# Performance work log

Hardware: AMD Instinct MI355X
Metric: run time of the kernel (lower is better)

## Reference

```python
import jax, jax.numpy as jnp
import numpy as np

NUM_LAYERS = 6
D_MODEL = 256
N_HEADS = 8
N_LEVELS = 4
N_POINTS = 4
D_FFN = 1024
HEAD_DIM = D_MODEL // N_HEADS
B = 2
NQ = 1600
SPATIAL = np.array([[64, 64], [32, 32], [16, 16], [8, 8]], dtype=np.int64)  # (H_l, W_l)
LEVEL_START = np.concatenate([[0], np.cumsum(SPATIAL.prod(1))[:-1]]).astype(np.int64)
S_TOTAL = int(SPATIAL.prod(1).sum())  # 5440


def layer_norm(x, g, b, eps=1e-5):
    mu = x.mean(-1, keepdims=True)
    var = ((x - mu) ** 2).mean(-1, keepdims=True)
    return (x - mu) * jax.lax.rsqrt(var + eps) * g + b


def mha(q, k, v, wq, bq, wk, bk, wv, bv, wo, bo):
    # torch nn.MultiheadAttention math (dropout=eval identity)
    Bb, N, d = q.shape
    def proj(x, w, bias):
        return (x @ w.T + bias).reshape(Bb, -1, N_HEADS, HEAD_DIM).transpose(0, 2, 1, 3)
    qh, kh, vh = proj(q, wq, bq), proj(k, wk, bk), proj(v, wv, bv)
    scores = jnp.einsum('bhqd,bhkd->bhqk', qh, kh) / np.float32(np.sqrt(HEAD_DIM))
    attn = jax.nn.softmax(scores, axis=-1)
    out = jnp.einsum('bhqk,bhkd->bhqd', attn, vh).transpose(0, 2, 1, 3).reshape(Bb, N, d)
    return out @ wo.T + bo


def ms_deform_attn(query, ref_points, src, w_off, b_off, w_attn, b_attn, w_val, b_val, w_out, b_out):
    Bb, Nq, d = query.shape
    value = (src @ w_val.T + b_val).reshape(Bb, -1, N_HEADS, HEAD_DIM)  # [B,S,H,D]
    off = (query @ w_off.T + b_off).reshape(Bb, Nq, N_HEADS, N_LEVELS, N_POINTS, 2)
    aw = (query @ w_attn.T + b_attn).reshape(Bb, Nq, N_HEADS, N_LEVELS * N_POINTS)
    aw = jax.nn.softmax(aw, -1).reshape(Bb, Nq, N_HEADS, N_LEVELS, N_POINTS)
    # offset normalizer is (W_l, H_l)
    norm = jnp.asarray(SPATIAL[:, ::-1].copy(), dtype=query.dtype)  # [L,2]
    loc = ref_points[:, :, None, :, None, :] + off / norm[None, None, None, :, None, :]
    out = jnp.zeros((Bb, Nq, N_HEADS, HEAD_DIM), query.dtype)
    for l in range(N_LEVELS):
        Hl, Wl = int(SPATIAL[l, 0]), int(SPATIAL[l, 1])
        s0 = int(LEVEL_START[l])
        v_l = value[:, s0:s0 + Hl * Wl].transpose(0, 2, 1, 3)  # [B,H,S_l,D]
        loc_l = loc[:, :, :, l]  # [B,Nq,H,P,2]
        # grid_sample bilinear, align_corners=False, padding zeros
        x = loc_l[..., 0] * Wl - 0.5
        y = loc_l[..., 1] * Hl - 0.5
        x0 = jnp.floor(x)
        y0 = jnp.floor(y)
        wx1 = x - x0
        wy1 = y - y0
        samp = jnp.zeros((Bb, Nq, N_HEADS, N_POINTS, HEAD_DIM), query.dtype)
        for dy, wy in ((0, 1.0 - wy1), (1, wy1)):
            for dx, wx in ((0, 1.0 - wx1), (1, wx1)):
                xi = x0 + dx
                yi = y0 + dy
                valid = ((xi >= 0) & (xi <= Wl - 1) & (yi >= 0) & (yi <= Hl - 1)).astype(query.dtype)
                xi_c = jnp.clip(xi, 0, Wl - 1).astype(jnp.int32)
                yi_c = jnp.clip(yi, 0, Hl - 1).astype(jnp.int32)
                idx = (yi_c * Wl + xi_c).transpose(0, 2, 1, 3).reshape(Bb, N_HEADS, Nq * N_POINTS)
                g = jnp.take_along_axis(v_l, idx[..., None], axis=2)  # [B,H,Nq*P,D]
                g = g.reshape(Bb, N_HEADS, Nq, N_POINTS, HEAD_DIM).transpose(0, 2, 1, 3, 4)
                samp = samp + g * (wx * wy * valid)[..., None]
        out = out + (samp * aw[:, :, :, l, :, None]).sum(3)
    return out.reshape(Bb, Nq, d) @ w_out.T + b_out


def decoder_forward(tgt, query_pos, reference_points, src, params):
    out = tgt
    for i in range(NUM_LAYERS):
        p = {k: v[i] for k, v in params.items()}
        q = out + query_pos
        t2 = mha(q, q, out, p['sa_w_q'], p['sa_b_q'], p['sa_w_k'], p['sa_b_k'],
                 p['sa_w_v'], p['sa_b_v'], p['sa_w_o'], p['sa_b_o'])
        out = layer_norm(out + t2, p['ln2_g'], p['ln2_b'])
        t2 = ms_deform_attn(out + query_pos, reference_points, src,
                            p['ca_w_off'], p['ca_b_off'], p['ca_w_attn'], p['ca_b_attn'],
                            p['ca_w_val'], p['ca_b_val'], p['ca_w_out'], p['ca_b_out'])
        out = out + t2
        out = layer_norm(out, p['ln1_g'], p['ln1_b'])
        t2 = jax.nn.relu(out @ p['ffn_w1'].T + p['ffn_b1']) @ p['ffn_w2'].T + p['ffn_b2']
        out = layer_norm(out + t2, p['ln3_g'], p['ln3_b'])
    return out


PARAM_NAMES = ['sa_w_q', 'sa_b_q', 'sa_w_k', 'sa_b_k', 'sa_w_v', 'sa_b_v', 'sa_w_o', 'sa_b_o',
               'ln2_g', 'ln2_b',
               'ca_w_off', 'ca_b_off', 'ca_w_attn', 'ca_b_attn', 'ca_w_val', 'ca_b_val',
               'ca_w_out', 'ca_b_out', 'ln1_g', 'ln1_b',
               'ffn_w1', 'ffn_b1', 'ffn_w2', 'ffn_b2', 'ln3_g', 'ln3_b']


def setup_inputs() -> dict:
    key = jax.random.key(0)
    ks = jax.random.split(key, 64)
    d = D_MODEL
    HLP = N_HEADS * N_LEVELS * N_POINTS
    shapes = {
        'sa_w_q': (d, d), 'sa_b_q': (d,), 'sa_w_k': (d, d), 'sa_b_k': (d,),
        'sa_w_v': (d, d), 'sa_b_v': (d,), 'sa_w_o': (d, d), 'sa_b_o': (d,),
        'ca_w_off': (HLP * 2, d), 'ca_b_off': (HLP * 2,),
        'ca_w_attn': (HLP, d), 'ca_b_attn': (HLP,),
        'ca_w_val': (d, d), 'ca_b_val': (d,),
        'ca_w_out': (d, d), 'ca_b_out': (d,),
        'ffn_w1': (D_FFN, d), 'ffn_b1': (D_FFN,),
        'ffn_w2': (d, D_FFN), 'ffn_b2': (D_FFN * 0 + d,) if False else (d,),
    }
    inp = {}
    inp['tgt'] = jax.random.normal(ks[0], (B, NQ, d), jnp.float32)
    inp['query_pos'] = jax.random.normal(ks[1], (B, NQ, d), jnp.float32)
    inp['reference_points'] = jax.random.uniform(ks[2], (B, NQ, N_LEVELS, 2), jnp.float32)
    inp['src'] = jax.random.normal(ks[3], (B, S_TOTAL, d), jnp.float32)
    i = 4
    for name in PARAM_NAMES:
        if name.startswith('ln'):
            if name.endswith('_g'):
                inp[name] = jnp.ones((NUM_LAYERS, d), jnp.float32)
            else:
                inp[name] = jnp.zeros((NUM_LAYERS, d), jnp.float32)
        else:
            shp = (NUM_LAYERS,) + shapes[name]
            inp[name] = jax.random.normal(ks[i], shp, jnp.float32) * 0.02
            i += 1
    inp['src_spatial_shapes'] = jnp.asarray(SPATIAL)
    inp['src_level_start_index'] = jnp.asarray(LEVEL_START)
    return inp


def reference(tgt, query_pos, reference_points, src,
              sa_w_q, sa_b_q, sa_w_k, sa_b_k, sa_w_v, sa_b_v, sa_w_o, sa_b_o,
              ln2_g, ln2_b,
              ca_w_off, ca_b_off, ca_w_attn, ca_b_attn, ca_w_val, ca_b_val,
              ca_w_out, ca_b_out, ln1_g, ln1_b,
              ffn_w1, ffn_b1, ffn_w2, ffn_b2, ln3_g, ln3_b,
              src_spatial_shapes, src_level_start_index):
    params = dict(zip(PARAM_NAMES, (sa_w_q, sa_b_q, sa_w_k, sa_b_k, sa_w_v, sa_b_v, sa_w_o, sa_b_o,
                                    ln2_g, ln2_b, ca_w_off, ca_b_off, ca_w_attn, ca_b_attn,
                                    ca_w_val, ca_b_val, ca_w_out, ca_b_out, ln1_g, ln1_b,
                                    ffn_w1, ffn_b1, ffn_w2, ffn_b2, ln3_g, ln3_b)))
    return decoder_forward(tgt, query_pos, reference_points, src, params)
```

## Files before the change

kernel.cpp:

```cpp
#include <hip/hip_runtime.h>

#define D_MODEL   256
#define NQ        1600
#define BATCH     2
#define NHEAD     8
#define HDIM      32
#define S_TOTAL   5440
#define D_FFN     1024
#define NUM_LAYERS 6

#define M_Q   (BATCH * NQ)
#define M_V   (BATCH * S_TOTAL)
#define ROW_ELEMS ((size_t)M_Q * D_MODEL)

using short8  = __attribute__((ext_vector_type(8))) short;
using floatx4 = __attribute__((ext_vector_type(4))) float;

__device__ __forceinline__ ushort f2bf(float f) {
    union { float f; unsigned u; } x; x.f = f;
    unsigned r = (x.u + 0x7fffu + ((x.u >> 16) & 1u)) >> 16;
    return (ushort)r;
}
__device__ __forceinline__ ushort f2bf_trunc(float f) {
    union { float f; unsigned u; } x; x.f = f;
    return (ushort)(x.u >> 16);
}
__device__ __forceinline__ float bf2f(ushort b) {
    union { unsigned u; float f; } x; x.u = ((unsigned)b) << 16;
    return x.f;
}

struct GSeg {
    const ushort* A;
    const ushort* W;
    const float*  bias;
    void*         C;
    int           ldc;
    int           mode;
    int           mblk;
    float         scale;
};
struct GArgs { GSeg s[16]; };

__global__ __launch_bounds__(256) void gemm_multi(GArgs args, int K)
{
    const GSeg sg = args.s[blockIdx.y];
    if ((int)blockIdx.x >= sg.mblk) return;
    __shared__ ushort Al[64][40];
    __shared__ ushort Bl[64][40];
    const int tid  = threadIdx.x;
    const int bm   = blockIdx.x * 64;
    const int lr   = tid >> 2;
    const int lc   = tid & 3;
    const int wave = tid >> 6;
    const int lane = tid & 63;
    const int mo   = (wave & 1) * 32;
    const int no   = (wave >> 1) * 32;
    const int row16 = lane & 15;
    const int quad  = lane >> 4;

    floatx4 acc[2][2] = {};

    const ushort* aG = sg.A + (size_t)(bm + lr) * K + lc * 8;
    const ushort* wG = sg.W + (size_t)lr * K + lc * 8;

    for (int k0 = 0; k0 < K; k0 += 32) {
        __syncthreads();
        *(short8*)&Al[lr][lc * 8] = *(const short8*)(aG + k0);
        *(short8*)&Bl[lr][lc * 8] = *(const short8*)(wG + k0);
        __syncthreads();
        short8 af0 = *(const short8*)&Al[mo + row16][quad * 8];
        short8 af1 = *(const short8*)&Al[mo + 16 + row16][quad * 8];
        short8 bf0 = *(const short8*)&Bl[no + row16][quad * 8];
        short8 bf1 = *(const short8*)&Bl[no + 16 + row16][quad * 8];
        acc[0][0] = __builtin_amdgcn_mfma_f32_16x16x32_bf16(af0, bf0, acc[0][0], 0, 0, 0);
        acc[0][1] = __builtin_amdgcn_mfma_f32_16x16x32_bf16(af0, bf1, acc[0][1], 0, 0, 0);
        acc[1][0] = __builtin_amdgcn_mfma_f32_16x16x32_bf16(af1, bf0, acc[1][0], 0, 0, 0);
        acc[1][1] = __builtin_amdgcn_mfma_f32_16x16x32_bf16(af1, bf1, acc[1][1], 0, 0, 0);
    }

#pragma unroll
    for (int mi = 0; mi < 2; ++mi)
#pragma unroll
        for (int ni = 0; ni < 2; ++ni) {
            const int col = no + ni * 16 + row16;
            const float bv = sg.bias[col];
            if (sg.mode == 3) {
                const int rowb = bm + mo + mi * 16 + quad * 4;
                const int b    = rowb / NQ;
                const int mloc = rowb - b * NQ;
                ushort4 st;
                st.x = f2bf((acc[mi][ni][0] + bv) * sg.scale);
                st.y = f2bf((acc[mi][ni][1] + bv) * sg.scale);
                st.z = f2bf((acc[mi][ni][2] + bv) * sg.scale);
                st.w = f2bf((acc[mi][ni][3] + bv) * sg.scale);
                *(ushort4*)((ushort*)sg.C + (size_t)b * (256 * NQ) + (size_t)col * NQ + mloc) = st;
            } else {
#pragma unroll
                for (int r = 0; r < 4; ++r) {
                    const int row = bm + mo + mi * 16 + quad * 4 + r;
                    float v = (acc[mi][ni][r] + bv) * sg.scale;
                    if (sg.mode == 0)
                        ((float*)sg.C)[(size_t)row * sg.ldc + col] = v;
                    else if (sg.mode == 1)
                        ((ushort*)sg.C)[(size_t)row * sg.ldc + col] = f2bf(fmaxf(v, 0.f));
                    else
                        ((ushort*)sg.C)[(size_t)row * sg.ldc + col] = f2bf(v);
                }
            }
        }
}

#define FSHIFT 16.0f

__global__ __launch_bounds__(256) void attn_mfma(const ushort* __restrict__ Qh,
                                                 const ushort* __restrict__ Kh,
                                                 const ushort* __restrict__ Vt,
                                                 ushort* __restrict__ Oh)
{
    const int bh = blockIdx.x;
    const int h  = bh & 7, b = bh >> 3;
    const int q0 = blockIdx.y * 16;
    const int tid  = threadIdx.x;
    const int wave = tid >> 6, lane = tid & 63;
    const int lr   = lane & 15, quad = lane >> 4;

    __shared__ ushort Pl[4][16][72];
    __shared__ float  Ol[4][16][33];
    __shared__ float  Ll[4][16];

    const ushort* Kb = Kh + (size_t)b * NQ * 256 + h * 32;
    const ushort* Vb = Vt + (size_t)bh * 32 * NQ;

    const short8 qf = *(const short8*)(Qh + (size_t)(b * NQ + q0 + lr) * 256 + h * 32 + quad * 8);

    float lsum[4] = {0.f, 0.f, 0.f, 0.f};
    floatx4 accO[2] = {};
    const floatx4 zero = {0.f, 0.f, 0.f, 0.f};

    for (int t = wave; t < NQ / 64; t += 4) {
        const int k0 = t * 64;
        floatx4 s[4];
#pragma unroll
        for (int cb = 0; cb < 4; ++cb) {
            const short8 kf = *(const short8*)(Kb + (size_t)(k0 + cb * 16 + lr) * 256 + quad * 8);
            s[cb] = __builtin_amdgcn_mfma_f32_16x16x32_bf16(qf, kf, zero, 0, 0, 0);
        }
#pragma unroll
        for (int cb = 0; cb < 4; ++cb)
#pragma unroll
            for (int r = 0; r < 4; ++r) {
                const float p = exp2f(fminf(s[cb][r], 100.f) - FSHIFT);
                lsum[r] += p;
                Pl[wave][quad * 4 + r][cb * 16 + lr] = f2bf_trunc(p);
            }
#pragma unroll
        for (int kc = 0; kc < 2; ++kc) {
            const short8 pf = *(const short8*)&Pl[wave][lr][kc * 32 + quad * 8];
            const short8 v0 = *(const short8*)(Vb + (size_t)lr * NQ + k0 + kc * 32 + quad * 8);
            const short8 v1 = *(const short8*)(Vb + (size_t)(16 + lr) * NQ + k0 + kc * 32 + quad * 8);
            accO[0] = __builtin_amdgcn_mfma_f32_16x16x32_bf16(pf, v0, accO[0], 0, 0, 0);
            accO[1] = __builtin_amdgcn_mfma_f32_16x16x32_bf16(pf, v1, accO[1], 0, 0, 0);
        }
    }

#pragma unroll
    for (int r = 0; r < 4; ++r) {
        float t = lsum[r];
        t += __shfl_xor(t, 1);
        t += __shfl_xor(t, 2);
        t += __shfl_xor(t, 4);
        t += __shfl_xor(t, 8);
        lsum[r] = t;
    }
#pragma unroll
    for (int r = 0; r < 4; ++r) {
        const int q = quad * 4 + r;
        Ol[wave][q][lr]      = accO[0][r];
        Ol[wave][q][16 + lr] = accO[1][r];
    }
    if (lr == 0) {
#pragma unroll
        for (int r = 0; r < 4; ++r) Ll[wave][quad * 4 + r] = lsum[r];
    }
    __syncthreads();

#pragma unroll
    for (int i = 0; i < 2; ++i) {
        const int idx = tid + i * 256;
        const int q = idx >> 5, d = idx & 31;
        const float o  = Ol[0][q][d] + Ol[1][q][d] + Ol[2][q][d] + Ol[3][q][d];
        const float lt = Ll[0][q] + Ll[1][q] + Ll[2][q] + Ll[3][q];
        Oh[(size_t)(b * NQ + q0 + q) * 256 + h * 32 + d] = f2bf(o / lt);
    }
}

struct CvtSeg { const float* in; ushort* out; int n4; };
struct CvtArgs { CvtSeg seg[11]; };

__global__ __launch_bounds__(256) void convert_kernel(CvtArgs args)
{
    const CvtSeg sg = args.seg[blockIdx.y];
    const int i = blockIdx.x * 256 + threadIdx.x;
    if (i < sg.n4) {
        float4 v = ((const float4*)sg.in)[i];
        ushort4 o;
        o.x = f2bf(v.x); o.y = f2bf(v.y); o.z = f2bf(v.z); o.w = f2bf(v.w);
        ((ushort4*)sg.out)[i] = o;
    }
}

__global__ __launch_bounds__(256) void init_out_kernel(const float* __restrict__ tgt,
                                                       const float* __restrict__ qpos,
                                                       float* __restrict__ out,
                                                       ushort* __restrict__ out_h,
                                                       ushort* __restrict__ qadd_h, int n4)
{
    const int i = blockIdx.x * 256 + threadIdx.x;
    if (i < n4) {
        float4 v = ((const float4*)tgt)[i];
        float4 p = ((const float4*)qpos)[i];
        ((float4*)out)[i] = v;
        ushort4 o, qa;
        o.x = f2bf(v.x); o.y = f2bf(v.y); o.z = f2bf(v.z); o.w = f2bf(v.w);
        qa.x = f2bf(v.x + p.x); qa.y = f2bf(v.y + p.y);
        qa.z = f2bf(v.z + p.z); qa.w = f2bf(v.w + p.w);
        ((ushort4*)out_h)[i] = o;
        ((ushort4*)qadd_h)[i] = qa;
    }
}

__global__ __launch_bounds__(256) void residual_ln_kernel(const float* __restrict__ x,
                                                          const float* __restrict__ t2,
                                                          const float* __restrict__ g,
                                                          const float* __restrict__ bt,
                                                          const float* __restrict__ qpos,
                                                          float* __restrict__ outp,
                                                          ushort* __restrict__ outp_h,
                                                          ushort* __restrict__ qadd_h)
{
    const int row = blockIdx.x;
    const int c = threadIdx.x;
    const size_t idx = (size_t)row * D_MODEL + c;
    float v = x[idx] + t2[idx];

    float s = v, s2 = v * v;
#pragma unroll
    for (int off = 32; off; off >>= 1) {
        s  += __shfl_xor(s,  off);
        s2 += __shfl_xor(s2, off);
    }
    __shared__ float ws[4], ws2[4];
    const int wid = c >> 6;
    if ((c & 63) == 0) { ws[wid] = s; ws2[wid] = s2; }
    __syncthreads();
    const float tot  = ws[0] + ws[1] + ws[2] + ws[3];
    const float tot2 = ws2[0] + ws2[1] + ws2[2] + ws2[3];
    const float mu  = tot * (1.f / 256.f);
    const float var = tot2 * (1.f / 256.f) - mu * mu;
    const float r = (v - mu) * rsqrtf(var + 1e-5f) * g[c] + bt[c];
    outp[idx] = r;
    outp_h[idx] = f2bf(r);
    qadd_h[idx] = f2bf(r + qpos[idx]);
}

__global__ __launch_bounds__(256) void sample_kernel(const ushort* __restrict__ value,
                                                     const float* __restrict__ off,
                                                     const float* __restrict__ aw,
                                                     const float* __restrict__ ref,
                                                     ushort* __restrict__ outp_h)
{
    const int bq = blockIdx.x;
    const int b  = bq / NQ;
    const int h  = threadIdx.x >> 5;
    const int c  = threadIdx.x & 31;

    const float* offrow = off + (size_t)bq * 256 + h * 32;
    const float* awrow  = aw  + (size_t)bq * 128 + h * 16;
    const float* refrow = ref + (size_t)bq * 8;

    float w16[16];
    {
        float mx = -1e30f;
#pragma unroll
        for (int i = 0; i < 16; ++i) { w16[i] = awrow[i]; mx = fmaxf(mx, w16[i]); }
        float sum = 0.f;
#pragma unroll
        for (int i = 0; i < 16; ++i) { w16[i] = __expf(w16[i] - mx); sum += w16[i]; }
        const float inv = 1.f / sum;
#pragma unroll
        for (int i = 0; i < 16; ++i) w16[i] *= inv;
    }

    const int HL[4]  = {64, 32, 16, 8};
    const int WLv[4] = {64, 32, 16, 8};
    const int S0[4]  = {0, 4096, 5120, 5376};

    float acc = 0.f;
#pragma unroll
    for (int l = 0; l < 4; ++l) {
        const int Hl = HL[l], Wl = WLv[l];
        const float rx = refrow[l * 2 + 0];
        const float ry = refrow[l * 2 + 1];
        const size_t lvl_base = ((size_t)b * S_TOTAL + S0[l]);
#pragma unroll
        for (int p = 0; p < 4; ++p) {
            const float ox = offrow[l * 8 + p * 2 + 0];
            const float oy = offrow[l * 8 + p * 2 + 1];
            const float w  = w16[l * 4 + p];
            const float locx = rx + ox / (float)Wl;
            const float locy = ry + oy / (float)Hl;
            const float x = locx * (float)Wl - 0.5f;
            const float y = locy * (float)Hl - 0.5f;
            const float x0f = floorf(x), y0f = floorf(y);
            const float wx1 = x - x0f, wy1 = y - y0f;
            const int x0 = (int)x0f, y0 = (int)y0f;
#pragma unroll
            for (int dy = 0; dy < 2; ++dy) {
                const int yi = y0 + dy;
                const float wy = dy ? wy1 : (1.f - wy1);
                const bool vy = (yi >= 0) && (yi <= Hl - 1);
                const int yc = min(max(yi, 0), Hl - 1);
#pragma unroll
                for (int dx = 0; dx < 2; ++dx) {
                    const int xi = x0 + dx;
                    const float wx = dx ? wx1 : (1.f - wx1);
                    const bool vx = (xi >= 0) && (xi <= Wl - 1);
                    const int xc = min(max(xi, 0), Wl - 1);
                    const float g = bf2f(value[((lvl_base + (size_t)yc * Wl + xc)) * 256 + h * 32 + c]);
                    acc += (vx && vy) ? g * (wx * wy * w) : 0.f;
                }
            }
        }
    }
    outp_h[(size_t)bq * D_MODEL + h * 32 + c] = f2bf(acc);
}

extern "C" void kernel_launch(void* const* d_in, const int* in_sizes, int n_in,
                              void* d_out, int out_size, void* d_ws, size_t ws_size,
                              hipStream_t stream)
{
    const float* tgt  = (const float*)d_in[0];
    const float* qpos = (const float*)d_in[1];
    const float* refp = (const float*)d_in[2];
    const float* src  = (const float*)d_in[3];

    float* bufT   = (float*)d_ws;
    float* bufOff = bufT   + ROW_ELEMS;
    float* bufAw  = bufOff + ROW_ELEMS;

    ushort* out_h   = (ushort*)(bufAw + (size_t)M_Q * 128);
    ushort* qadd_h  = out_h   + ROW_ELEMS;
    ushort* bufX_h  = qadd_h  + ROW_ELEMS;
    ushort* bufQh   = bufX_h  + ROW_ELEMS;
    ushort* bufKh   = bufQh   + ROW_ELEMS;
    ushort* bufVt   = bufKh   + ROW_ELEMS;
    ushort* bufF_h  = bufVt   + ROW_ELEMS;
    ushort* bufVal  = bufF_h  + (size_t)M_Q * D_FFN;
    ushort* src_h   = bufVal  + (size_t)M_V * D_MODEL;
    ushort* wpool   = src_h   + (size_t)M_V * D_MODEL;

    ushort* wq_h    = wpool;
    ushort* wk_h    = wq_h    + 393216;
    ushort* wv_h    = wk_h    + 393216;
    ushort* wo_h    = wv_h    + 393216;
    ushort* woff_h  = wo_h    + 393216;
    ushort* wattn_h = woff_h  + 393216;
    ushort* wval_h  = wattn_h + 196608;
    ushort* wout_h  = wval_h  + 393216;
    ushort* w1_h    = wout_h  + 393216;
    ushort* w2_h    = w1_h    + 1572864;

    float* out = (float*)d_out;

    CvtArgs ca;
    ca.seg[0]  = { src,                    src_h,   (int)((size_t)M_V * D_MODEL / 4) };
    ca.seg[1]  = { (const float*)d_in[4],  wq_h,    393216 / 4 };
    ca.seg[2]  = { (const float*)d_in[6],  wk_h,    393216 / 4 };
    ca.seg[3]  = { (const float*)d_in[8],  wv_h,    393216 / 4 };
    ca.seg[4]  = { (const float*)d_in[10], wo_h,    393216 / 4 };
    ca.seg[5]  = { (const float*)d_in[14], woff_h,  393216 / 4 };
    ca.seg[6]  = { (const float*)d_in[16], wattn_h, 196608 / 4 };
    ca.seg[7]  = { (const float*)d_in[18], wval_h,  393216 / 4 };
    ca.seg[8]  = { (const float*)d_in[20], wout_h,  393216 / 4 };
    ca.seg[9]  = { (const float*)d_in[24], w1_h,    1572864 / 4 };
    ca.seg[10] = { (const float*)d_in[26], w2_h,    1572864 / 4 };
    convert_kernel<<<dim3(2720, 11), 256, 0, stream>>>(ca);

    init_out_kernel<<<800, 256, 0, stream>>>(tgt, qpos, out, out_h, qadd_h, (int)(ROW_ELEMS / 4));

    const float QSCALE = 0.1767766952966369f * 1.4426950408889634f;
    const int MB_Q = M_Q / 64;
    const int MB_V = M_V / 64;

    for (int l = 0; l < NUM_LAYERS; ++l) {
        const float* sa_b_q    = (const float*)d_in[5]  + (size_t)l * 256;
        const float* sa_b_k    = (const float*)d_in[7]  + (size_t)l * 256;
        const float* sa_b_v    = (const float*)d_in[9]  + (size_t)l * 256;
        const float* sa_b_o    = (const float*)d_in[11] + (size_t)l * 256;
        const float* ln2_g     = (const float*)d_in[12] + (size_t)l * 256;
        const float* ln2_b     = (const float*)d_in[13] + (size_t)l * 256;
        const float* ca_b_off  = (const float*)d_in[15] + (size_t)l * 256;
        const float* ca_b_attn = (const float*)d_in[17] + (size_t)l * 128;
        const float* ca_b_val  = (const float*)d_in[19] + (size_t)l * 256;
        const float* ca_b_out  = (const float*)d_in[21] + (size_t)l * 256;
        const float* ln1_g     = (const float*)d_in[22] + (size_t)l * 256;
        const float* ln1_b     = (const float*)d_in[23] + (size_t)l * 256;
        const float* ffn_b1    = (const float*)d_in[25] + (size_t)l * 1024;
        const float* ffn_b2    = (const float*)d_in[27] + (size_t)l * 256;
        const float* ln3_g     = (const float*)d_in[28] + (size_t)l * 256;
        const float* ln3_b     = (const float*)d_in[29] + (size_t)l * 256;

        const ushort* wq = wq_h    + (size_t)l * 65536;
        const ushort* wk = wk_h    + (size_t)l * 65536;
        const ushort* wv = wv_h    + (size_t)l * 65536;
        const ushort* wo = wo_h    + (size_t)l * 65536;
        const ushort* wf = woff_h  + (size_t)l * 65536;
        const ushort* wa = wattn_h + (size_t)l * 32768;
        const ushort* wl = wval_h  + (size_t)l * 65536;
        const ushort* wu = wout_h  + (size_t)l * 65536;
        const ushort* w1 = w1_h    + (size_t)l * 262144;
        const ushort* w2 = w2_h    + (size_t)l * 262144;

        GArgs ga;

        for (int i = 0; i < 4; ++i) {
            ga.s[i]      = { qadd_h, wq + (size_t)i * 64 * 256, sa_b_q + i * 64, bufQh + i * 64, 256, 2, MB_Q, QSCALE };
            ga.s[4 + i]  = { qadd_h, wk + (size_t)i * 64 * 256, sa_b_k + i * 64, bufKh + i * 64, 256, 2, MB_Q, 1.f };
            ga.s[8 + i]  = { out_h,  wv + (size_t)i * 64 * 256, sa_b_v + i * 64, bufVt + (size_t)i * 64 * NQ, 256, 3, MB_Q, 1.f };
            ga.s[12 + i] = { src_h,  wl + (size_t)i * 64 * 256, ca_b_val + i * 64, bufVal + i * 64, 256, 2, MB_V, 1.f };
        }
        gemm_multi<<<dim3(MB_V, 16), 256, 0, stream>>>(ga, 256);

        attn_mfma<<<dim3(16, NQ / 16), 256, 0, stream>>>(bufQh, bufKh, bufVt, bufX_h);

        for (int i = 0; i < 4; ++i)
            ga.s[i] = { bufX_h, wo + (size_t)i * 64 * 256, sa_b_o + i * 64, bufT + i * 64, 256, 0, MB_Q, 1.f };
        gemm_multi<<<dim3(MB_Q, 4), 256, 0, stream>>>(ga, 256);

        residual_ln_kernel<<<M_Q, 256, 0, stream>>>(out, bufT, ln2_g, ln2_b, qpos, out, out_h, qadd_h);

        for (int i = 0; i < 4; ++i)
            ga.s[i] = { qadd_h, wf + (size_t)i * 64 * 256, ca_b_off + i * 64, bufOff + i * 64, 256, 0, MB_Q, 1.f };
        for (int i = 0; i < 2; ++i)
            ga.s[4 + i] = { qadd_h, wa + (size_t)i * 64 * 256, ca_b_attn + i * 64, bufAw + i * 64, 128, 0, MB_Q, 1.f };
        gemm_multi<<<dim3(MB_Q, 6), 256, 0, stream>>>(ga, 256);

        sample_kernel<<<M_Q, 256, 0, stream>>>(bufVal, bufOff, bufAw, refp, bufX_h);

        for (int i = 0; i < 4; ++i)
            ga.s[i] = { bufX_h, wu + (size_t)i * 64 * 256, ca_b_out + i * 64, bufT + i * 64, 256, 0, MB_Q, 1.f };
        gemm_multi<<<dim3(MB_Q, 4), 256, 0, stream>>>(ga, 256);

        residual_ln_kernel<<<M_Q, 256, 0, stream>>>(out, bufT, ln1_g, ln1_b, qpos, out, out_h, qadd_h);

        for (int i = 0; i < 16; ++i)
            ga.s[i] = { out_h, w1 + (size_t)i * 64 * 256, ffn_b1 + i * 64, bufF_h + i * 64, 1024, 1, MB_Q, 1.f };
        gemm_multi<<<dim3(MB_Q, 16), 256, 0, stream>>>(ga, 256);

        for (int i = 0; i < 4; ++i)
            ga.s[i] = { bufF_h, w2 + (size_t)i * 64 * 1024, ffn_b2 + i * 64, bufT + i * 64, 256, 0, MB_Q, 1.f };
        gemm_multi<<<dim3(MB_Q, 4), 256, 0, stream>>>(ga, 1024);

        residual_ln_kernel<<<M_Q, 256, 0, stream>>>(out, bufT, ln3_g, ln3_b, qpos, out, out_h, qadd_h);
    }

    (void)in_sizes; (void)n_in; (void)out_size; (void)ws_size;
}
```

Measured before the change: 1.038 ms.

## Fuse output GEMMs with residual LayerNorm and keep attention probabilities in registers

Result: slower. 1.305 ms (+25.8%).

```diff
diff --git a/kernel.cpp b/kernel.cpp
--- a/kernel.cpp
+++ b/kernel.cpp
@@ -14,7 +14,20 @@
 #define ROW_ELEMS ((size_t)M_Q * D_MODEL)
 
 using short8  = __attribute__((ext_vector_type(8))) short;
+using short4v = __attribute__((ext_vector_type(4))) short;
 using floatx4 = __attribute__((ext_vector_type(4))) float;
+
+#if __has_builtin(__builtin_amdgcn_mfma_f32_16x16x16_bf16)
+  #define MFMA16K16(a,b,c) __builtin_amdgcn_mfma_f32_16x16x16_bf16((a),(b),(c),0,0,0)
+#else
+  #define MFMA16K16(a,b,c) __builtin_amdgcn_mfma_f32_16x16x16bf16_1k((a),(b),(c),0,0,0)
+#endif
+
+#if __has_builtin(__builtin_amdgcn_exp2f)
+  #define EXP2F(x) __builtin_amdgcn_exp2f(x)
+#else
+  #define EXP2F(x) exp2f(x)
+#endif
 
 __device__ __forceinline__ ushort f2bf(float f) {
     union { float f; unsigned u; } x; x.f = f;
@@ -111,6 +124,106 @@
         }
 }
 
+__global__ __launch_bounds__(256) void gemm_ln(const ushort* __restrict__ A,
+                                               const ushort* __restrict__ W,
+                                               const float* __restrict__ bias,
+                                               const float* __restrict__ g,
+                                               const float* __restrict__ bt,
+                                               const float* __restrict__ qpos,
+                                               const float* __restrict__ resid,
+                                               float* __restrict__ outp,
+                                               ushort* __restrict__ outp_h,
+                                               ushort* __restrict__ qadd_h,
+                                               int K)
+{
+    __shared__ ushort St[320][40];
+    __shared__ float  R1[4][64], R2[4][64];
+    const int tid  = threadIdx.x;
+    const int bm   = blockIdx.x * 64;
+    const int wave = tid >> 6, lane = tid & 63;
+    const int lr   = lane & 15, quad = lane >> 4;
+
+    floatx4 acc[4][4] = {};
+
+    for (int k0 = 0; k0 < K; k0 += 32) {
+        __syncthreads();
+#pragma unroll
+        for (int i = 0; i < 5; ++i) {
+            const int c = tid + i * 256;
+            const int row = c >> 2, kc = c & 3;
+            const ushort* src = (row < 64)
+                ? (A + (size_t)(bm + row) * K + k0 + kc * 8)
+                : (W + (size_t)(row - 64) * K + k0 + kc * 8);
+            *(short8*)&St[row][kc * 8] = *(const short8*)src;
+        }
+        __syncthreads();
+        short8 af[4], bf[4];
+#pragma unroll
+        for (int mg = 0; mg < 4; ++mg) af[mg] = *(const short8*)&St[mg * 16 + lr][quad * 8];
+#pragma unroll
+        for (int ng = 0; ng < 4; ++ng) bf[ng] = *(const short8*)&St[64 + wave * 64 + ng * 16 + lr][quad * 8];
+#pragma unroll
+        for (int mg = 0; mg < 4; ++mg)
+#pragma unroll
+            for (int ng = 0; ng < 4; ++ng)
+                acc[mg][ng] = __builtin_amdgcn_mfma_f32_16x16x32_bf16(af[mg], bf[ng], acc[mg][ng], 0, 0, 0);
+    }
+
+#pragma unroll
+    for (int mg = 0; mg < 4; ++mg)
+#pragma unroll
+        for (int ng = 0; ng < 4; ++ng) {
+            const int col = wave * 64 + ng * 16 + lr;
+            const float bv = bias[col];
+#pragma unroll
+            for (int r = 0; r < 4; ++r) {
+                const int row = bm + mg * 16 + quad * 4 + r;
+                acc[mg][ng][r] += bv + resid[(size_t)row * 256 + col];
+            }
+        }
+
+#pragma unroll
+    for (int mg = 0; mg < 4; ++mg)
+#pragma unroll
+        for (int r = 0; r < 4; ++r) {
+            float s1 = acc[mg][0][r] + acc[mg][1][r] + acc[mg][2][r] + acc[mg][3][r];
+            float s2 = acc[mg][0][r]*acc[mg][0][r] + acc[mg][1][r]*acc[mg][1][r]
+                     + acc[mg][2][r]*acc[mg][2][r] + acc[mg][3][r]*acc[mg][3][r];
+            s1 += __shfl_xor(s1, 1); s2 += __shfl_xor(s2, 1);
+            s1 += __shfl_xor(s1, 2); s2 += __shfl_xor(s2, 2);
+            s1 += __shfl_xor(s1, 4); s2 += __shfl_xor(s2, 4);
+            s1 += __shfl_xor(s1, 8); s2 += __shfl_xor(s2, 8);
+            if (lr == 0) {
+                const int rl = mg * 16 + quad * 4 + r;
+                R1[wave][rl] = s1;
+                R2[wave][rl] = s2;
+            }
+        }
+    __syncthreads();
+
+#pragma unroll
+    for (int mg = 0; mg < 4; ++mg)
+#pragma unroll
+        for (int r = 0; r < 4; ++r) {
+            const int rl = mg * 16 + quad * 4 + r;
+            const float tot1 = R1[0][rl] + R1[1][rl] + R1[2][rl] + R1[3][rl];
+            const float tot2 = R2[0][rl] + R2[1][rl] + R2[2][rl] + R2[3][rl];
+            const float mu  = tot1 * (1.f / 256.f);
+            const float var = tot2 * (1.f / 256.f) - mu * mu;
+            const float rs  = rsqrtf(var + 1e-5f);
+            const int row = bm + rl;
+#pragma unroll
+            for (int ng = 0; ng < 4; ++ng) {
+                const int col = wave * 64 + ng * 16 + lr;
+                const size_t idx = (size_t)row * 256 + col;
+                const float rv = (acc[mg][ng][r] - mu) * rs * g[col] + bt[col];
+                outp[idx]   = rv;
+                outp_h[idx] = f2bf(rv);
+                qadd_h[idx] = f2bf(rv + qpos[idx]);
+            }
+        }
+}
+
 #define FSHIFT 16.0f
 
 __global__ __launch_bounds__(256) void attn_mfma(const ushort* __restrict__ Qh,
@@ -125,63 +238,46 @@
     const int wave = tid >> 6, lane = tid & 63;
     const int lr   = lane & 15, quad = lane >> 4;
 
-    __shared__ ushort Pl[4][16][72];
-    __shared__ float  Ol[4][16][33];
-    __shared__ float  Ll[4][16];
+    __shared__ float Ol[4][16][33];
+    __shared__ float Ll[4][16];
 
     const ushort* Kb = Kh + (size_t)b * NQ * 256 + h * 32;
     const ushort* Vb = Vt + (size_t)bh * 32 * NQ;
 
     const short8 qf = *(const short8*)(Qh + (size_t)(b * NQ + q0 + lr) * 256 + h * 32 + quad * 8);
 
-    float lsum[4] = {0.f, 0.f, 0.f, 0.f};
+    float lsum = 0.f;
     floatx4 accO[2] = {};
     const floatx4 zero = {0.f, 0.f, 0.f, 0.f};
 
     for (int t = wave; t < NQ / 64; t += 4) {
         const int k0 = t * 64;
-        floatx4 s[4];
 #pragma unroll
         for (int cb = 0; cb < 4; ++cb) {
             const short8 kf = *(const short8*)(Kb + (size_t)(k0 + cb * 16 + lr) * 256 + quad * 8);
-            s[cb] = __builtin_amdgcn_mfma_f32_16x16x32_bf16(qf, kf, zero, 0, 0, 0);
-        }
-#pragma unroll
-        for (int cb = 0; cb < 4; ++cb)
+            const floatx4 st = __builtin_amdgcn_mfma_f32_16x16x32_bf16(kf, qf, zero, 0, 0, 0);
+            short4v pf;
 #pragma unroll
             for (int r = 0; r < 4; ++r) {
-                const float p = exp2f(fminf(s[cb][r], 100.f) - FSHIFT);
-                lsum[r] += p;
-                Pl[wave][quad * 4 + r][cb * 16 + lr] = f2bf_trunc(p);
+                const float p = EXP2F(fminf(st[r], 100.f) - FSHIFT);
+                lsum += p;
+                pf[r] = (short)f2bf_trunc(p);
             }
-#pragma unroll
-        for (int kc = 0; kc < 2; ++kc) {
-            const short8 pf = *(const short8*)&Pl[wave][lr][kc * 32 + quad * 8];
-            const short8 v0 = *(const short8*)(Vb + (size_t)lr * NQ + k0 + kc * 32 + quad * 8);
-            const short8 v1 = *(const short8*)(Vb + (size_t)(16 + lr) * NQ + k0 + kc * 32 + quad * 8);
-            accO[0] = __builtin_amdgcn_mfma_f32_16x16x32_bf16(pf, v0, accO[0], 0, 0, 0);
-            accO[1] = __builtin_amdgcn_mfma_f32_16x16x32_bf16(pf, v1, accO[1], 0, 0, 0);
-        }
-    }
-
-#pragma unroll
-    for (int r = 0; r < 4; ++r) {
-        float t = lsum[r];
-        t += __shfl_xor(t, 1);
-        t += __shfl_xor(t, 2);
-        t += __shfl_xor(t, 4);
-        t += __shfl_xor(t, 8);
-        lsum[r] = t;
-    }
+            const short4v v0 = *(const short4v*)(Vb + (size_t)lr * NQ + k0 + cb * 16 + quad * 4);
+            const short4v v1 = *(const short4v*)(Vb + (size_t)(16 + lr) * NQ + k0 + cb * 16 + quad * 4);
+            accO[0] = MFMA16K16(pf, v0, accO[0]);
+            accO[1] = MFMA16K16(pf, v1, accO[1]);
+        }
+    }
+
+    lsum += __shfl_xor(lsum, 16);
+    lsum += __shfl_xor(lsum, 32);
+    if (quad == 0) Ll[wave][lr] = lsum;
 #pragma unroll
     for (int r = 0; r < 4; ++r) {
         const int q = quad * 4 + r;
         Ol[wave][q][lr]      = accO[0][r];
         Ol[wave][q][16 + lr] = accO[1][r];
-    }
-    if (lr == 0) {
-#pragma unroll
-        for (int r = 0; r < 4; ++r) Ll[wave][quad * 4 + r] = lsum[r];
     }
     __syncthreads();
 
@@ -230,40 +326,6 @@
     }
 }
 
-__global__ __launch_bounds__(256) void residual_ln_kernel(const float* __restrict__ x,
-                                                          const float* __restrict__ t2,
-                                                          const float* __restrict__ g,
-                                                          const float* __restrict__ bt,
-                                                          const float* __restrict__ qpos,
-                                                          float* __restrict__ outp,
-                                                          ushort* __restrict__ outp_h,
-                                                          ushort* __restrict__ qadd_h)
-{
-    const int row = blockIdx.x;
-    const int c = threadIdx.x;
-    const size_t idx = (size_t)row * D_MODEL + c;
-    float v = x[idx] + t2[idx];
-
-    float s = v, s2 = v * v;
-#pragma unroll
-    for (int off = 32; off; off >>= 1) {
-        s  += __shfl_xor(s,  off);
-        s2 += __shfl_xor(s2, off);
-    }
-    __shared__ float ws[4], ws2[4];
-    const int wid = c >> 6;
-    if ((c & 63) == 0) { ws[wid] = s; ws2[wid] = s2; }
-    __syncthreads();
-    const float tot  = ws[0] + ws[1] + ws[2] + ws[3];
-    const float tot2 = ws2[0] + ws2[1] + ws2[2] + ws2[3];
-    const float mu  = tot * (1.f / 256.f);
-    const float var = tot2 * (1.f / 256.f) - mu * mu;
-    const float r = (v - mu) * rsqrtf(var + 1e-5f) * g[c] + bt[c];
-    outp[idx] = r;
-    outp_h[idx] = f2bf(r);
-    qadd_h[idx] = f2bf(r + qpos[idx]);
-}
-
 __global__ __launch_bounds__(256) void sample_kernel(const ushort* __restrict__ value,
                                                      const float* __restrict__ off,
                                                      const float* __restrict__ aw,
@@ -327,8 +389,8 @@
                     const float wx = dx ? wx1 : (1.f - wx1);
                     const bool vx = (xi >= 0) && (xi <= Wl - 1);
                     const int xc = min(max(xi, 0), Wl - 1);
-                    const float g = bf2f(value[((lvl_base + (size_t)yc * Wl + xc)) * 256 + h * 32 + c]);
-                    acc += (vx && vy) ? g * (wx * wy * w) : 0.f;
+                    const float gv = bf2f(value[((lvl_base + (size_t)yc * Wl + xc)) * 256 + h * 32 + c]);
+                    acc += (vx && vy) ? gv * (wx * wy * w) : 0.f;
                 }
             }
         }
@@ -345,8 +407,7 @@
     const float* refp = (const float*)d_in[2];
     const float* src  = (const float*)d_in[3];
 
-    float* bufT   = (float*)d_ws;
-    float* bufOff = bufT   + ROW_ELEMS;
+    float* bufOff = (float*)d_ws;
     float* bufAw  = bufOff + ROW_ELEMS;
 
     ushort* out_h   = (ushort*)(bufAw + (size_t)M_Q * 128);
@@ -434,11 +495,8 @@
 
         attn_mfma<<<dim3(16, NQ / 16), 256, 0, stream>>>(bufQh, bufKh, bufVt, bufX_h);
 
-        for (int i = 0; i < 4; ++i)
-            ga.s[i] = { bufX_h, wo + (size_t)i * 64 * 256, sa_b_o + i * 64, bufT + i * 64, 256, 0, MB_Q, 1.f };
-        gemm_multi<<<dim3(MB_Q, 4), 256, 0, stream>>>(ga, 256);
-
-        residual_ln_kernel<<<M_Q, 256, 0, stream>>>(out, bufT, ln2_g, ln2_b, qpos, out, out_h, qadd_h);
+        gemm_ln<<<MB_Q, 256, 0, stream>>>(bufX_h, wo, sa_b_o, ln2_g, ln2_b, qpos,
+                                          out, out, out_h, qadd_h, 256);
 
         for (int i = 0; i < 4; ++i)
             ga.s[i] = { qadd_h, wf + (size_t)i * 64 * 256, ca_b_off + i * 64, bufOff + i * 64, 256, 0, MB_Q, 1.f };
@@ -448,21 +506,15 @@
 
         sample_kernel<<<M_Q, 256, 0, stream>>>(bufVal, bufOff, bufAw, refp, bufX_h);
 
-        for (int i = 0; i < 4; ++i)
-            ga.s[i] = { bufX_h, wu + (size_t)i * 64 * 256, ca_b_out + i * 64, bufT + i * 64, 256, 0, MB_Q, 1.f };
-        gemm_multi<<<dim3(MB_Q, 4), 256, 0, stream>>>(ga, 256);
-
-        residual_ln_kernel<<<M_Q, 256, 0, stream>>>(out, bufT, ln1_g, ln1_b, qpos, out, out_h, qadd_h);
+        gemm_ln<<<MB_Q, 256, 0, stream>>>(bufX_h, wu, ca_b_out, ln1_g, ln1_b, qpos,
+                                          out, out, out_h, qadd_h, 256);
 
         for (int i = 0; i < 16; ++i)
             ga.s[i] = { out_h, w1 + (size_t)i * 64 * 256, ffn_b1 + i * 64, bufF_h + i * 64, 1024, 1, MB_Q, 1.f };
         gemm_multi<<<dim3(MB_Q, 16), 256, 0, stream>>>(ga, 256);
 
-        for (int i = 0; i < 4; ++i)
-            ga.s[i] = { bufF_h, w2 + (size_t)i * 64 * 1024, ffn_b2 + i * 64, bufT + i * 64, 256, 0, MB_Q, 1.f };
-        gemm_multi<<<dim3(MB_Q, 4), 256, 0, stream>>>(ga, 1024);
-
-        residual_ln_kernel<<<M_Q, 256, 0, stream>>>(out, bufT, ln3_g, ln3_b, qpos, out, out_h, qadd_h);
+        gemm_ln<<<MB_Q, 256, 0, stream>>>(bufF_h, w2, ffn_b2, ln3_g, ln3_b, qpos,
+                                          out, out, out_h, qadd_h, 1024);
     }
 
     (void)in_sizes; (void)n_in; (void)out_size; (void)ws_size;
```

## Keep attention probabilities in registers and prefetch next K/V tiles

Applied to the files above, without the earlier changes.

New measurement: 1.127 ms. 1.09x slower.

```diff
diff --git a/kernel.cpp b/kernel.cpp
--- a/kernel.cpp
+++ b/kernel.cpp
@@ -14,7 +14,20 @@
 #define ROW_ELEMS ((size_t)M_Q * D_MODEL)
 
 using short8  = __attribute__((ext_vector_type(8))) short;
+using short4v = __attribute__((ext_vector_type(4))) short;
 using floatx4 = __attribute__((ext_vector_type(4))) float;
+
+#if __has_builtin(__builtin_amdgcn_mfma_f32_16x16x16_bf16)
+  #define MFMA16K16(a,b,c) __builtin_amdgcn_mfma_f32_16x16x16_bf16((a),(b),(c),0,0,0)
+#else
+  #define MFMA16K16(a,b,c) __builtin_amdgcn_mfma_f32_16x16x16bf16_1k((a),(b),(c),0,0,0)
+#endif
+
+#if __has_builtin(__builtin_amdgcn_exp2f)
+  #define EXP2F(x) __builtin_amdgcn_exp2f(x)
+#else
+  #define EXP2F(x) exp2f(x)
+#endif
 
 __device__ __forceinline__ ushort f2bf(float f) {
     union { float f; unsigned u; } x; x.f = f;
@@ -125,63 +138,69 @@
     const int wave = tid >> 6, lane = tid & 63;
     const int lr   = lane & 15, quad = lane >> 4;
 
-    __shared__ ushort Pl[4][16][72];
-    __shared__ float  Ol[4][16][33];
-    __shared__ float  Ll[4][16];
+    __shared__ float Ol[4][16][33];
+    __shared__ float Ll[4][16];
 
     const ushort* Kb = Kh + (size_t)b * NQ * 256 + h * 32;
     const ushort* Vb = Vt + (size_t)bh * 32 * NQ;
 
     const short8 qf = *(const short8*)(Qh + (size_t)(b * NQ + q0 + lr) * 256 + h * 32 + quad * 8);
 
-    float lsum[4] = {0.f, 0.f, 0.f, 0.f};
+    float lsum = 0.f;
     floatx4 accO[2] = {};
     const floatx4 zero = {0.f, 0.f, 0.f, 0.f};
 
-    for (int t = wave; t < NQ / 64; t += 4) {
-        const int k0 = t * 64;
-        floatx4 s[4];
+    const int NT = NQ / 64;
+    int t = wave;
+
+    short8  kf[4];
+    short4v v0[4], v1[4];
+#pragma unroll
+    for (int cb = 0; cb < 4; ++cb) {
+        kf[cb] = *(const short8*)(Kb + (size_t)(t * 64 + cb * 16 + lr) * 256 + quad * 8);
+        v0[cb] = *(const short4v*)(Vb + (size_t)lr * NQ        + t * 64 + cb * 16 + quad * 4);
+        v1[cb] = *(const short4v*)(Vb + (size_t)(16 + lr) * NQ + t * 64 + cb * 16 + quad * 4);
+    }
+
+    while (true) {
+        const int tn = (t + 4 < NT) ? (t + 4) : t;
+        short8  kfn[4];
+        short4v v0n[4], v1n[4];
 #pragma unroll
         for (int cb = 0; cb < 4; ++cb) {
-            const short8 kf = *(const short8*)(Kb + (size_t)(k0 + cb * 16 + lr) * 256 + quad * 8);
-            s[cb] = __builtin_amdgcn_mfma_f32_16x16x32_bf16(qf, kf, zero, 0, 0, 0);
+            kfn[cb] = *(const short8*)(Kb + (size_t)(tn * 64 + cb * 16 + lr) * 256 + quad * 8);
+            v0n[cb] = *(const short4v*)(Vb + (size_t)lr * NQ        + tn * 64 + cb * 16 + quad * 4);
+            v1n[cb] = *(const short4v*)(Vb + (size_t)(16 + lr) * NQ + tn * 64 + cb * 16 + quad * 4);
         }
-#pragma unroll
-        for (int cb = 0; cb < 4; ++cb)
+
+#pragma unroll
+        for (int cb = 0; cb < 4; ++cb) {
+            const floatx4 st = __builtin_amdgcn_mfma_f32_16x16x32_bf16(kf[cb], qf, zero, 0, 0, 0);
+            short4v pf;
 #pragma unroll
             for (int r = 0; r < 4; ++r) {
-                const float p = exp2f(fminf(s[cb][r], 100.f) - FSHIFT);
-                lsum[r] += p;
-                Pl[wave][quad * 4 + r][cb * 16 + lr] = f2bf_trunc(p);
+                const float p = EXP2F(fminf(st[r], 100.f) - FSHIFT);
+                lsum += p;
+                pf[r] = (short)f2bf_trunc(p);
             }
-#pragma unroll
-        for (int kc = 0; kc < 2; ++kc) {
-            const short8 pf = *(const short8*)&Pl[wave][lr][kc * 32 + quad * 8];
-            const short8 v0 = *(const short8*)(Vb + (size_t)lr * NQ + k0 + kc * 32 + quad * 8);
-            const short8 v1 = *(const short8*)(Vb + (size_t)(16 + lr) * NQ + k0 + kc * 32 + quad * 8);
-            accO[0] = __builtin_amdgcn_mfma_f32_16x16x32_bf16(pf, v0, accO[0], 0, 0, 0);
-            accO[1] = __builtin_amdgcn_mfma_f32_16x16x32_bf16(pf, v1, accO[1], 0, 0, 0);
+            accO[0] = MFMA16K16(pf, v0[cb], accO[0]);
+            accO[1] = MFMA16K16(pf, v1[cb], accO[1]);
         }
-    }
-
-#pragma unroll
-    for (int r = 0; r < 4; ++r) {
-        float t = lsum[r];
-        t += __shfl_xor(t, 1);
-        t += __shfl_xor(t, 2);
-        t += __shfl_xor(t, 4);
-        t += __shfl_xor(t, 8);
-        lsum[r] = t;
-    }
+
+        if (t + 4 >= NT) break;
+        t += 4;
+#pragma unroll
+        for (int cb = 0; cb < 4; ++cb) { kf[cb] = kfn[cb]; v0[cb] = v0n[cb]; v1[cb] = v1n[cb]; }
+    }
+
+    lsum += __shfl_xor(lsum, 16);
+    lsum += __shfl_xor(lsum, 32);
+    if (quad == 0) Ll[wave][lr] = lsum;
 #pragma unroll
     for (int r = 0; r < 4; ++r) {
         const int q = quad * 4 + r;
         Ol[wave][q][lr]      = accO[0][r];
         Ol[wave][q][16 + lr] = accO[1][r];
-    }
-    if (lr == 0) {
-#pragma unroll
-        for (int r = 0; r < 4; ++r) Ll[wave][quad * 4 + r] = lsum[r];
     }
     __syncthreads();
 
@@ -327,8 +346,8 @@
                     const float wx = dx ? wx1 : (1.f - wx1);
                     const bool vx = (xi >= 0) && (xi <= Wl - 1);
                     const int xc = min(max(xi, 0), Wl - 1);
-                    const float g = bf2f(value[((lvl_base + (size_t)yc * Wl + xc)) * 256 + h * 32 + c]);
-                    acc += (vx && vy) ? g * (wx * wy * w) : 0.f;
+                    const float gv = bf2f(value[((lvl_base + (size_t)yc * Wl + xc)) * 256 + h * 32 + c]);
+                    acc += (vx && vy) ? gv * (wx * wy * w) : 0.f;
                 }
             }
         }
```
